# Kernel tuning notes

Measured on AMD Instinct MI355X. Metric: run time of the kernel, lower is better.

## Reference

```python
import jax, jax.numpy as jnp
import numpy as np

E, H, F = 8, 1024, 2048   # experts, hidden, ffn
B, S = 1, 1024
JITTER = 0.01             # router_jitter_noise


def setup_inputs() -> dict:
    key = jax.random.key(0)
    ks = jax.random.split(key, 5)
    return {
        "hidden_states": jax.random.normal(ks[0], (B, S, H), jnp.float32),
        "gate_w": jax.random.normal(ks[1], (E, H), jnp.float32) * 0.02,
        "w1": jax.random.normal(ks[2], (E, F, H), jnp.float32) * 0.02,
        "w2": jax.random.normal(ks[3], (E, H, F), jnp.float32) * 0.02,
        "w3": jax.random.normal(ks[4], (E, F, H), jnp.float32) * 0.02,
    }


def _sparsemixer_eval(scores, jitter_eps):
    # scores: [T, E]. Inference path of sparsemixer (training=False).
    T = scores.shape[0]
    rows = jnp.arange(T)
    # top-1
    max1 = jnp.max(scores, axis=-1, keepdims=True)
    sel1 = jnp.argmax(scores, axis=-1)
    factor1 = jnp.maximum(jnp.abs(scores), max1)          # scores.abs().clamp(min=max1)
    mask1 = (max1 - scores) / factor1 > 2.0 * jitter_eps
    gates1 = jax.nn.softmax(jnp.where(mask1, -jnp.inf, scores), axis=-1)
    mult1 = gates1[rows, sel1]
    # top-2: mask out the top-1 expert
    masked_scores = scores.at[rows, sel1].set(-jnp.inf)
    max2 = jnp.max(masked_scores, axis=-1, keepdims=True)
    sel2 = jnp.argmax(masked_scores, axis=-1)
    factor2 = jnp.maximum(jnp.abs(scores), max2)
    mask2 = (max2 - scores) / factor2 > 2.0 * jitter_eps
    gates2 = jax.nn.softmax(jnp.where(mask2, -jnp.inf, masked_scores), axis=-1)
    mult2 = gates2[rows, sel2]
    multiplier = jnp.stack([mult1, mult2], axis=-1)       # [T, 2]
    selected = jnp.stack([sel1, sel2], axis=-1)           # [T, 2]
    return multiplier, selected


def reference(hidden_states, gate_w, w1, w2, w3):
    b, s, h = hidden_states.shape
    x = hidden_states.reshape(-1, h)                      # [T, H]
    router_logits = x @ gate_w.T                          # [T, E]
    mult, sel = _sparsemixer_eval(router_logits, JITTER)
    n_exp = gate_w.shape[0]
    # combined routing weight per (token, expert): sum of top-k multipliers
    weight = jnp.sum(mult[..., None] * jax.nn.one_hot(sel, n_exp, dtype=x.dtype), axis=1)  # [T, E]
    # dense masked dispatch: evaluate every expert, combine with routing weights
    h1 = jnp.einsum('th,efh->etf', x, w1)                 # [E, T, F]
    h3 = jnp.einsum('th,efh->etf', x, w3)
    inter = jax.nn.silu(h1) * h3
    out_e = jnp.einsum('etf,ehf->eth', inter, w2)         # [E, T, H]
    final = jnp.einsum('eth,te->th', out_e, weight)       # [T, H]
    return final.reshape(b, s, h), router_logits
```

## Files before the change

kernel.cpp:

```cpp
#include <hip/hip_runtime.h>
#include <hip/hip_bf16.h>
#include <math.h>


#define T_TOK 1024
#define H_DIM 1024
#define F_DIM 2048
#define N_EXP 8
#define JIT 0.01f

#define BK  64
#define LDK 68
#define NK1 (H_DIM / BK)
#define NK2 (F_DIM / BK)
#define MT_MAX 24

typedef __bf16 bf16_t;
typedef __bf16 bf16x8 __attribute__((ext_vector_type(8)));
typedef __bf16 bf16x4 __attribute__((ext_vector_type(4)));
typedef float f32x4 __attribute__((ext_vector_type(4)));

__device__ inline bf16x4 cvt4(float4 v) {
    bf16x4 r;
    r[0] = (bf16_t)v.x; r[1] = (bf16_t)v.y; r[2] = (bf16_t)v.z; r[3] = (bf16_t)v.w;
    return r;
}

#define WS_CNT   0
#define WS_BASE  64
#define WS_TOK   128
#define WS_WGT   (128 + 32768)
#define WS_SLOT  (WS_WGT + 32768)
#define WS_INTER 131072
#define WS_ACC   (131072 + 8388608)

__global__ __launch_bounds__(256) void router_k(
    const float* __restrict__ x, const float* __restrict__ gw,
    float* __restrict__ logits_out,
    int* __restrict__ cnt, int* __restrict__ tok,
    float* __restrict__ wgt, int* __restrict__ slot)
{
    int wave = threadIdx.x >> 6, lane = threadIdx.x & 63;
    int t = blockIdx.x * 4 + wave;
    const float* xr = x + (size_t)t * H_DIM;
    int h0 = lane * 16;

    float acc[N_EXP];
#pragma unroll
    for (int e = 0; e < N_EXP; e++) acc[e] = 0.f;
#pragma unroll
    for (int j = 0; j < 16; j += 4) {
        float4 xv = *(const float4*)(xr + h0 + j);
#pragma unroll
        for (int e = 0; e < N_EXP; e++) {
            float4 gv = *(const float4*)(gw + e * H_DIM + h0 + j);
            acc[e] += xv.x * gv.x + xv.y * gv.y + xv.z * gv.z + xv.w * gv.w;
        }
    }
#pragma unroll
    for (int m = 32; m > 0; m >>= 1)
#pragma unroll
        for (int e = 0; e < N_EXP; e++) acc[e] += __shfl_xor(acc[e], m, 64);

    if (lane == 0) {
        float s[N_EXP];
#pragma unroll
        for (int e = 0; e < N_EXP; e++) {
            s[e] = acc[e];
            logits_out[t * N_EXP + e] = s[e];
        }
        float max1 = -INFINITY; int sel1 = 0;
        for (int e = 0; e < N_EXP; e++) if (s[e] > max1) { max1 = s[e]; sel1 = e; }
        float denom1 = 0.f;
        for (int e = 0; e < N_EXP; e++) {
            float factor = fmaxf(fabsf(s[e]), max1);
            bool m = ((max1 - s[e]) / factor) > (2.0f * JIT);
            if (!m) denom1 += expf(s[e] - max1);
        }
        float mult1 = 1.0f / denom1;
        float max2 = -INFINITY; int sel2 = 0;
        for (int e = 0; e < N_EXP; e++)
            if (e != sel1 && s[e] > max2) { max2 = s[e]; sel2 = e; }
        float denom2 = 0.f;
        for (int e = 0; e < N_EXP; e++) {
            if (e == sel1) continue;
            float factor = fmaxf(fabsf(s[e]), max2);
            bool m = ((max2 - s[e]) / factor) > (2.0f * JIT);
            if (!m) denom2 += expf(s[e] - max2);
        }
        float mult2 = 1.0f / denom2;

        int p1 = atomicAdd(&cnt[sel1], 1);
        tok[sel1 * T_TOK + p1] = t; wgt[sel1 * T_TOK + p1] = mult1; slot[sel1 * T_TOK + p1] = 0;
        int p2 = atomicAdd(&cnt[sel2], 1);
        tok[sel2 * T_TOK + p2] = t; wgt[sel2 * T_TOK + p2] = mult2; slot[sel2 * T_TOK + p2] = 1;
    }
}

__global__ void prefix_k(const int* __restrict__ cnt, int* __restrict__ base)
{
    if (threadIdx.x == 0 && blockIdx.x == 0) {
        int a = 0;
        for (int e = 0; e < N_EXP; e++) { base[e] = a; a += cnt[e]; }
    }
}

__global__ __launch_bounds__(256, 2) void gemm1_k(
    const float* __restrict__ x,
    const float* __restrict__ w1,
    const float* __restrict__ w3,
    const int* __restrict__ cnt, const int* __restrict__ base,
    const int* __restrict__ tok,
    bf16_t* __restrict__ inter)
{
    int mt = blockIdx.x >> 5;
    int nt = blockIdx.x & 31;
    int e = 0, m0 = 0, found = 0, accb = 0;
#pragma unroll
    for (int ee = 0; ee < N_EXP; ee++) {
        int b = (cnt[ee] + 127) >> 7;
        if (!found && mt < accb + b) { e = ee; m0 = (mt - accb) << 7; found = 1; }
        accb += b;
    }
    if (!found) return;
    int cntE = cnt[e];
    int n0 = nt * 64;
    int tid = threadIdx.x;
    int lane = tid & 63, quad = lane >> 4, l16 = lane & 15;
    int wave = tid >> 6;

    __shared__ __align__(16) bf16_t Al[2][128 * LDK];
    __shared__ __align__(16) bf16_t B1l[2][64 * LDK];
    __shared__ __align__(16) bf16_t B3l[2][64 * LDK];
    __shared__ int tokL[128];

    if (tid < 128) {
        int r = m0 + tid;
        tokL[tid] = tok[e * T_TOK + (r < cntE ? r : cntE - 1)];
    }
    __syncthreads();

    int rA[8], kA[8], ofsA[8];
#pragma unroll
    for (int i = 0; i < 8; i++) {
        int c = tid + i * 256;
        rA[i] = c >> 4; kA[i] = c & 15;
        ofsA[i] = tokL[rA[i]] * H_DIM + kA[i] * 4;
    }
    int rB[4], kB[4], ofsB[4];
    const float* w1e = w1 + (size_t)e * F_DIM * H_DIM;
    const float* w3e = w3 + (size_t)e * F_DIM * H_DIM;
#pragma unroll
    for (int i = 0; i < 4; i++) {
        int c = tid + i * 256;
        rB[i] = c >> 4; kB[i] = c & 15;
        ofsB[i] = (n0 + rB[i]) * H_DIM + kB[i] * 4;
    }

    f32x4 acc1[2][4], acc3[2][4];
#pragma unroll
    for (int fi = 0; fi < 2; fi++)
#pragma unroll
        for (int fj = 0; fj < 4; fj++) {
            acc1[fi][fj] = f32x4{0.f, 0.f, 0.f, 0.f};
            acc3[fi][fj] = f32x4{0.f, 0.f, 0.f, 0.f};
        }

    float4 pA[8], p1[4], p3[4];
#pragma unroll
    for (int i = 0; i < 8; i++) pA[i] = *(const float4*)(x + ofsA[i]);
#pragma unroll
    for (int i = 0; i < 4; i++) {
        p1[i] = *(const float4*)(w1e + ofsB[i]);
        p3[i] = *(const float4*)(w3e + ofsB[i]);
    }

#pragma unroll 2
    for (int kk = 0; kk < NK1; kk++) {
        const int cur = kk & 1;
#pragma unroll
        for (int i = 0; i < 8; i++)
            *(bf16x4*)&Al[cur][rA[i] * LDK + kA[i] * 4] = cvt4(pA[i]);
#pragma unroll
        for (int i = 0; i < 4; i++) {
            *(bf16x4*)&B1l[cur][rB[i] * LDK + kB[i] * 4] = cvt4(p1[i]);
            *(bf16x4*)&B3l[cur][rB[i] * LDK + kB[i] * 4] = cvt4(p3[i]);
        }
        __syncthreads();
        if (kk + 1 < NK1) {
            const int k0 = (kk + 1) * BK;
#pragma unroll
            for (int i = 0; i < 8; i++) pA[i] = *(const float4*)(x + ofsA[i] + k0);
#pragma unroll
            for (int i = 0; i < 4; i++) {
                p1[i] = *(const float4*)(w1e + ofsB[i] + k0);
                p3[i] = *(const float4*)(w3e + ofsB[i] + k0);
            }
        }
#pragma unroll
        for (int s = 0; s < 2; s++) {
            int ko = s * 32 + quad * 8;
            bf16x8 af[2], b1f[4], b3f[4];
#pragma unroll
            for (int fi = 0; fi < 2; fi++)
                af[fi] = *(const bf16x8*)&Al[cur][(wave * 32 + fi * 16 + l16) * LDK + ko];
#pragma unroll
            for (int fj = 0; fj < 4; fj++) {
                b1f[fj] = *(const bf16x8*)&B1l[cur][(fj * 16 + l16) * LDK + ko];
                b3f[fj] = *(const bf16x8*)&B3l[cur][(fj * 16 + l16) * LDK + ko];
            }
#pragma unroll
            for (int fi = 0; fi < 2; fi++)
#pragma unroll
                for (int fj = 0; fj < 4; fj++) {
                    acc1[fi][fj] = __builtin_amdgcn_mfma_f32_16x16x32_bf16(af[fi], b1f[fj], acc1[fi][fj], 0, 0, 0);
                    acc3[fi][fj] = __builtin_amdgcn_mfma_f32_16x16x32_bf16(af[fi], b3f[fj], acc3[fi][fj], 0, 0, 0);
                }
        }
    }

    int rowBase = base[e];
#pragma unroll
    for (int fi = 0; fi < 2; fi++)
#pragma unroll
        for (int fj = 0; fj < 4; fj++) {
            int ff = n0 + fj * 16 + l16;
#pragma unroll
            for (int r = 0; r < 4; r++) {
                int mm = m0 + wave * 32 + fi * 16 + quad * 4 + r;
                if (mm < cntE) {
                    float h1 = acc1[fi][fj][r], h3 = acc3[fi][fj][r];
                    float v = (h1 / (1.f + expf(-h1))) * h3;
                    inter[(size_t)(rowBase + mm) * F_DIM + ff] = (bf16_t)v;
                }
            }
        }
}

__global__ __launch_bounds__(256, 3) void gemm2_k(
    const bf16_t* __restrict__ inter,
    const float* __restrict__ w2,
    const int* __restrict__ cnt, const int* __restrict__ base,
    const int* __restrict__ tok,
    const float* __restrict__ wgt, const int* __restrict__ slot,
    float* __restrict__ accOut)
{
    int mt = blockIdx.x >> 4;
    int nt = blockIdx.x & 15;
    int e = 0, m0 = 0, found = 0, accb = 0;
#pragma unroll
    for (int ee = 0; ee < N_EXP; ee++) {
        int b = (cnt[ee] + 127) >> 7;
        if (!found && mt < accb + b) { e = ee; m0 = (mt - accb) << 7; found = 1; }
        accb += b;
    }
    if (!found) return;
    int cntE = cnt[e];
    int n0 = nt * 64;
    int tid = threadIdx.x;
    int lane = tid & 63, quad = lane >> 4, l16 = lane & 15;
    int wave = tid >> 6;
    int rowBase = base[e];

    __shared__ __align__(16) bf16_t Al[2][128 * LDK];
    __shared__ __align__(16) bf16_t Bl[2][64 * LDK];

    int rA[4], kA[4], ofsA[4];
#pragma unroll
    for (int i = 0; i < 4; i++) {
        int c = tid + i * 256;
        rA[i] = c >> 3; kA[i] = c & 7;
        int row = m0 + rA[i]; if (row >= cntE) row = cntE - 1;
        ofsA[i] = (rowBase + row) * F_DIM + kA[i] * 8;
    }
    int rB[4], kB[4], ofsB[4];
    const float* w2e = w2 + (size_t)e * H_DIM * F_DIM;
#pragma unroll
    for (int i = 0; i < 4; i++) {
        int c = tid + i * 256;
        rB[i] = c >> 4; kB[i] = c & 15;
        ofsB[i] = (n0 + rB[i]) * F_DIM + kB[i] * 4;
    }

    f32x4 acc[2][4];
#pragma unroll
    for (int fi = 0; fi < 2; fi++)
#pragma unroll
        for (int fj = 0; fj < 4; fj++) acc[fi][fj] = f32x4{0.f, 0.f, 0.f, 0.f};

    bf16x8 pa[4];
    float4 pb[4];
#pragma unroll
    for (int i = 0; i < 4; i++) {
        pa[i] = *(const bf16x8*)(inter + ofsA[i]);
        pb[i] = *(const float4*)(w2e + ofsB[i]);
    }

#pragma unroll 2
    for (int kk = 0; kk < NK2; kk++) {
        const int cur = kk & 1;
#pragma unroll
        for (int i = 0; i < 4; i++) {
            *(bf16x8*)&Al[cur][rA[i] * LDK + kA[i] * 8] = pa[i];
            *(bf16x4*)&Bl[cur][rB[i] * LDK + kB[i] * 4] = cvt4(pb[i]);
        }
        __syncthreads();
        if (kk + 1 < NK2) {
            const int k0 = (kk + 1) * BK;
#pragma unroll
            for (int i = 0; i < 4; i++) {
                pa[i] = *(const bf16x8*)(inter + ofsA[i] + k0);
                pb[i] = *(const float4*)(w2e + ofsB[i] + k0);
            }
        }
#pragma unroll
        for (int s = 0; s < 2; s++) {
            int ko = s * 32 + quad * 8;
            bf16x8 af[2], bfr[4];
#pragma unroll
            for (int fi = 0; fi < 2; fi++)
                af[fi] = *(const bf16x8*)&Al[cur][(wave * 32 + fi * 16 + l16) * LDK + ko];
#pragma unroll
            for (int fj = 0; fj < 4; fj++)
                bfr[fj] = *(const bf16x8*)&Bl[cur][(fj * 16 + l16) * LDK + ko];
#pragma unroll
            for (int fi = 0; fi < 2; fi++)
#pragma unroll
                for (int fj = 0; fj < 4; fj++)
                    acc[fi][fj] = __builtin_amdgcn_mfma_f32_16x16x32_bf16(af[fi], bfr[fj], acc[fi][fj], 0, 0, 0);
        }
    }

#pragma unroll
    for (int fi = 0; fi < 2; fi++)
#pragma unroll
        for (int r = 0; r < 4; r++) {
            int mm = m0 + wave * 32 + fi * 16 + quad * 4 + r;
            if (mm < cntE) {
                int t = tok[e * T_TOK + mm];
                float wv = wgt[e * T_TOK + mm];
                int sl = slot[e * T_TOK + mm];
                float* dst = accOut + (size_t)sl * T_TOK * H_DIM + (size_t)t * H_DIM;
#pragma unroll
                for (int fj = 0; fj < 4; fj++)
                    dst[n0 + fj * 16 + l16] = acc[fi][fj][r] * wv;
            }
        }
}

__global__ __launch_bounds__(256) void combine_k(const float* __restrict__ acc,
                                                 float* __restrict__ out)
{
    int i = blockIdx.x * 256 + threadIdx.x;
    const float4* a0 = (const float4*)acc;
    const float4* a1 = (const float4*)(acc + (size_t)T_TOK * H_DIM);
    float4 v0 = a0[i];
    float4 v1 = a1[i];
    float4 r;
    r.x = v0.x + v1.x; r.y = v0.y + v1.y; r.z = v0.z + v1.z; r.w = v0.w + v1.w;
    ((float4*)out)[i] = r;
}

extern "C" void kernel_launch(void* const* d_in, const int* in_sizes, int n_in,
                              void* d_out, int out_size, void* d_ws, size_t ws_size,
                              hipStream_t stream) {
    const float* x  = (const float*)d_in[0];
    const float* gw = (const float*)d_in[1];
    const float* w1 = (const float*)d_in[2];
    const float* w2 = (const float*)d_in[3];
    const float* w3 = (const float*)d_in[4];
    float* out = (float*)d_out;
    float* logits_out = out + (size_t)T_TOK * H_DIM;

    char* ws = (char*)d_ws;
    int*    cnt   = (int*)(ws + WS_CNT);
    int*    basep = (int*)(ws + WS_BASE);
    int*    tok   = (int*)(ws + WS_TOK);
    float*  wgt   = (float*)(ws + WS_WGT);
    int*    slot  = (int*)(ws + WS_SLOT);
    bf16_t* inter = (bf16_t*)(ws + WS_INTER);
    float*  accO  = (float*)(ws + WS_ACC);

    hipMemsetAsync(cnt, 0, 64, stream);
    router_k<<<T_TOK / 4, 256, 0, stream>>>(x, gw, logits_out, cnt, tok, wgt, slot);
    prefix_k<<<1, 64, 0, stream>>>(cnt, basep);
    gemm1_k<<<dim3(MT_MAX * 32), 256, 0, stream>>>(x, w1, w3, cnt, basep, tok, inter);
    gemm2_k<<<dim3(MT_MAX * 16), 256, 0, stream>>>(inter, w2, cnt, basep, tok, wgt, slot, accO);
    combine_k<<<(T_TOK * H_DIM / 4) / 256, 256, 0, stream>>>(accO, out);
}
```

Before: 314.5 us.

## Stream fp32 weights to LDS via global_load_lds with 4-stage pipeline

Both expert GEMMs now load fp32 weight tiles straight into LDS with global_load_lds, in a four-buffer pipeline that runs two tiles ahead. Each tile is converted to bf16 when read from LDS rather than before storing. Activations (x, inter) are register-prefetched two steps ahead, loaded per wave directly in MFMA fragment layout instead of being staged in LDS. The wave layout changes to a 2x2 grid with 64x32 tiles per wave, and BK drops to 32. gemm2's occupancy hint goes from 3 to 2. The goal is to cut LDS store traffic and register staging and to overlap memory with MFMA, at the cost of hand-tuned vmcnt waits and more LDS use per block.

Measured after the change: 430.8 us. 37.0% more time.

```diff
diff --git a/kernel.cpp b/kernel.cpp
--- a/kernel.cpp
+++ b/kernel.cpp
@@ -9,21 +9,26 @@
 #define N_EXP 8
 #define JIT 0.01f
 
-#define BK  64
-#define LDK 68
+#define BK  32
 #define NK1 (H_DIM / BK)
 #define NK2 (F_DIM / BK)
 #define MT_MAX 24
 
 typedef __bf16 bf16_t;
 typedef __bf16 bf16x8 __attribute__((ext_vector_type(8)));
-typedef __bf16 bf16x4 __attribute__((ext_vector_type(4)));
 typedef float f32x4 __attribute__((ext_vector_type(4)));
 
-__device__ inline bf16x4 cvt4(float4 v) {
-    bf16x4 r;
-    r[0] = (bf16_t)v.x; r[1] = (bf16_t)v.y; r[2] = (bf16_t)v.z; r[3] = (bf16_t)v.w;
+__device__ inline bf16x8 cvt8(float4 a, float4 b) {
+    bf16x8 r;
+    r[0] = (bf16_t)a.x; r[1] = (bf16_t)a.y; r[2] = (bf16_t)a.z; r[3] = (bf16_t)a.w;
+    r[4] = (bf16_t)b.x; r[5] = (bf16_t)b.y; r[6] = (bf16_t)b.z; r[7] = (bf16_t)b.w;
     return r;
+}
+
+__device__ inline void gl16(const float* g, float* l) {
+    __builtin_amdgcn_global_load_lds(
+        (const __attribute__((address_space(1))) unsigned int*)g,
+        (__attribute__((address_space(3))) unsigned int*)l, 16, 0, 0);
 }
 
 #define WS_CNT   0
@@ -128,10 +133,12 @@
     int tid = threadIdx.x;
     int lane = tid & 63, quad = lane >> 4, l16 = lane & 15;
     int wave = tid >> 6;
-
-    __shared__ __align__(16) bf16_t Al[2][128 * LDK];
-    __shared__ __align__(16) bf16_t B1l[2][64 * LDK];
-    __shared__ __align__(16) bf16_t B3l[2][64 * LDK];
+    int wm = wave >> 1, wn = wave & 1;
+
+    __shared__ __align__(16) float Bl0[4096];
+    __shared__ __align__(16) float Bl1[4096];
+    __shared__ __align__(16) float Bl2[4096];
+    __shared__ __align__(16) float Bl3[4096];
     __shared__ int tokL[128];
 
     if (tid < 128) {
@@ -140,96 +147,102 @@
     }
     __syncthreads();
 
-    int rA[8], kA[8], ofsA[8];
-#pragma unroll
-    for (int i = 0; i < 8; i++) {
-        int c = tid + i * 256;
-        rA[i] = c >> 4; kA[i] = c & 15;
-        ofsA[i] = tokL[rA[i]] * H_DIM + kA[i] * 4;
-    }
-    int rB[4], kB[4], ofsB[4];
     const float* w1e = w1 + (size_t)e * F_DIM * H_DIM;
     const float* w3e = w3 + (size_t)e * F_DIM * H_DIM;
-#pragma unroll
-    for (int i = 0; i < 4; i++) {
-        int c = tid + i * 256;
-        rB[i] = c >> 4; kB[i] = c & 15;
-        ofsB[i] = (n0 + rB[i]) * H_DIM + kB[i] * 4;
-    }
-
-    f32x4 acc1[2][4], acc3[2][4];
-#pragma unroll
-    for (int fi = 0; fi < 2; fi++)
-#pragma unroll
-        for (int fj = 0; fj < 4; fj++) {
+
+    const float* srcB[4];
+    int dstF[4];
+#pragma unroll
+    for (int j = 0; j < 4; j++) {
+        int g = wave * 4 + j;
+        int mat = g >> 3, fj = (g >> 1) & 3, h = g & 1;
+        srcB[j] = (mat ? w3e : w1e) + (size_t)(n0 + fj * 16 + l16) * H_DIM + quad * 8 + h * 4;
+        dstF[j] = mat * 2048 + fj * 512 + h * 256;
+    }
+
+    int aoff[4];
+#pragma unroll
+    for (int fi = 0; fi < 4; fi++)
+        aoff[fi] = tokL[wm * 64 + fi * 16 + l16] * H_DIM + quad * 8;
+
+    f32x4 acc1[4][2], acc3[4][2];
+#pragma unroll
+    for (int fi = 0; fi < 4; fi++)
+#pragma unroll
+        for (int fj = 0; fj < 2; fj++) {
             acc1[fi][fj] = f32x4{0.f, 0.f, 0.f, 0.f};
             acc3[fi][fj] = f32x4{0.f, 0.f, 0.f, 0.f};
         }
 
-    float4 pA[8], p1[4], p3[4];
-#pragma unroll
-    for (int i = 0; i < 8; i++) pA[i] = *(const float4*)(x + ofsA[i]);
-#pragma unroll
-    for (int i = 0; i < 4; i++) {
-        p1[i] = *(const float4*)(w1e + ofsB[i]);
-        p3[i] = *(const float4*)(w3e + ofsB[i]);
-    }
-
-#pragma unroll 2
-    for (int kk = 0; kk < NK1; kk++) {
-        const int cur = kk & 1;
-#pragma unroll
-        for (int i = 0; i < 8; i++)
-            *(bf16x4*)&Al[cur][rA[i] * LDK + kA[i] * 4] = cvt4(pA[i]);
-#pragma unroll
-        for (int i = 0; i < 4; i++) {
-            *(bf16x4*)&B1l[cur][rB[i] * LDK + kB[i] * 4] = cvt4(p1[i]);
-            *(bf16x4*)&B3l[cur][rB[i] * LDK + kB[i] * 4] = cvt4(p3[i]);
-        }
-        __syncthreads();
-        if (kk + 1 < NK1) {
-            const int k0 = (kk + 1) * BK;
-#pragma unroll
-            for (int i = 0; i < 8; i++) pA[i] = *(const float4*)(x + ofsA[i] + k0);
-#pragma unroll
-            for (int i = 0; i < 4; i++) {
-                p1[i] = *(const float4*)(w1e + ofsB[i] + k0);
-                p3[i] = *(const float4*)(w3e + ofsB[i] + k0);
-            }
-        }
-#pragma unroll
-        for (int s = 0; s < 2; s++) {
-            int ko = s * 32 + quad * 8;
-            bf16x8 af[2], b1f[4], b3f[4];
-#pragma unroll
-            for (int fi = 0; fi < 2; fi++)
-                af[fi] = *(const bf16x8*)&Al[cur][(wave * 32 + fi * 16 + l16) * LDK + ko];
-#pragma unroll
-            for (int fj = 0; fj < 4; fj++) {
-                b1f[fj] = *(const bf16x8*)&B1l[cur][(fj * 16 + l16) * LDK + ko];
-                b3f[fj] = *(const bf16x8*)&B3l[cur][(fj * 16 + l16) * LDK + ko];
-            }
-#pragma unroll
-            for (int fi = 0; fi < 2; fi++)
-#pragma unroll
-                for (int fj = 0; fj < 4; fj++) {
-                    acc1[fi][fj] = __builtin_amdgcn_mfma_f32_16x16x32_bf16(af[fi], b1f[fj], acc1[fi][fj], 0, 0, 0);
-                    acc3[fi][fj] = __builtin_amdgcn_mfma_f32_16x16x32_bf16(af[fi], b3f[fj], acc3[fi][fj], 0, 0, 0);
-                }
-        }
-    }
+    float4 pa[2][4][2];
+
+#define G1_ISSUE_B(T, WR)                                                   \
+    { _Pragma("unroll") for (int j = 0; j < 4; j++)                         \
+          gl16(srcB[j] + (T) * 32, WR + dstF[j]); }
+
+#define G1_ISSUE_A(T, PAR)                                                  \
+    { _Pragma("unroll") for (int fi = 0; fi < 4; fi++) {                    \
+          pa[PAR][fi][0] = *(const float4*)(x + aoff[fi] + (T) * 32);       \
+          pa[PAR][fi][1] = *(const float4*)(x + aoff[fi] + (T) * 32 + 4); } }
+
+#define G1_SYNC(N)                                                          \
+    __builtin_amdgcn_sched_barrier(0);                                      \
+    asm volatile("s_waitcnt vmcnt(" #N ")" ::: "memory");                   \
+    __builtin_amdgcn_s_barrier();                                           \
+    __builtin_amdgcn_sched_barrier(0);
+
+#define G1_COMPUTE(KK, PAR, RD, DO_A)                                       \
+    {                                                                       \
+        bf16x8 af[4];                                                       \
+        _Pragma("unroll") for (int fi = 0; fi < 4; fi++)                    \
+            af[fi] = cvt8(pa[PAR][fi][0], pa[PAR][fi][1]);                  \
+        if (DO_A) { G1_ISSUE_A((KK) + 2, PAR); }                            \
+        _Pragma("unroll") for (int fjl = 0; fjl < 2; fjl++) {               \
+            int fb = (wn * 2 + fjl) * 512 + lane * 4;                       \
+            float4 u1 = *(const float4*)(RD + fb);                          \
+            float4 v1 = *(const float4*)(RD + fb + 256);                    \
+            float4 u3 = *(const float4*)(RD + 2048 + fb);                   \
+            float4 v3 = *(const float4*)(RD + 2048 + fb + 256);             \
+            bf16x8 b1 = cvt8(u1, v1), b3 = cvt8(u3, v3);                    \
+            _Pragma("unroll") for (int fi = 0; fi < 4; fi++) {              \
+                acc1[fi][fjl] = __builtin_amdgcn_mfma_f32_16x16x32_bf16(af[fi], b1, acc1[fi][fjl], 0, 0, 0); \
+                acc3[fi][fjl] = __builtin_amdgcn_mfma_f32_16x16x32_bf16(af[fi], b3, acc3[fi][fjl], 0, 0, 0); \
+            }                                                               \
+        }                                                                   \
+    }
+
+#define G1_BODY(KK, PAR, WR, RD, N, DO_B, DO_A)                             \
+    { if (DO_B) { G1_ISSUE_B((KK) + 2, WR); }                               \
+      G1_SYNC(N)                                                            \
+      G1_COMPUTE(KK, PAR, RD, DO_A) }
+
+    G1_ISSUE_B(0, Bl0);
+    G1_ISSUE_A(0, 0);
+    G1_ISSUE_B(1, Bl1);
+    G1_ISSUE_A(1, 1);
+
+    for (int kb = 0; kb < 28; kb += 4) {
+        G1_BODY(kb + 0, 0, Bl2, Bl0, 16, 1, 1)
+        G1_BODY(kb + 1, 1, Bl3, Bl1, 16, 1, 1)
+        G1_BODY(kb + 2, 0, Bl0, Bl2, 16, 1, 1)
+        G1_BODY(kb + 3, 1, Bl1, Bl3, 16, 1, 1)
+    }
+    G1_BODY(28, 0, Bl2, Bl0, 16, 1, 1)
+    G1_BODY(29, 1, Bl3, Bl1, 16, 1, 1)
+    G1_BODY(30, 0, Bl0, Bl2, 12, 0, 0)
+    G1_BODY(31, 1, Bl1, Bl3, 0, 0, 0)
 
     int rowBase = base[e];
 #pragma unroll
-    for (int fi = 0; fi < 2; fi++)
-#pragma unroll
-        for (int fj = 0; fj < 4; fj++) {
-            int ff = n0 + fj * 16 + l16;
+    for (int fi = 0; fi < 4; fi++)
+#pragma unroll
+        for (int fjl = 0; fjl < 2; fjl++) {
+            int ff = n0 + wn * 32 + fjl * 16 + l16;
 #pragma unroll
             for (int r = 0; r < 4; r++) {
-                int mm = m0 + wave * 32 + fi * 16 + quad * 4 + r;
+                int mm = m0 + wm * 64 + fi * 16 + quad * 4 + r;
                 if (mm < cntE) {
-                    float h1 = acc1[fi][fj][r], h3 = acc3[fi][fj][r];
+                    float h1 = acc1[fi][fjl][r], h3 = acc3[fi][fjl][r];
                     float v = (h1 / (1.f + expf(-h1))) * h3;
                     inter[(size_t)(rowBase + mm) * F_DIM + ff] = (bf16_t)v;
                 }
@@ -237,7 +250,7 @@
         }
 }
 
-__global__ __launch_bounds__(256, 3) void gemm2_k(
+__global__ __launch_bounds__(256, 2) void gemm2_k(
     const bf16_t* __restrict__ inter,
     const float* __restrict__ w2,
     const int* __restrict__ cnt, const int* __restrict__ base,
@@ -260,90 +273,99 @@
     int tid = threadIdx.x;
     int lane = tid & 63, quad = lane >> 4, l16 = lane & 15;
     int wave = tid >> 6;
+    int wm = wave >> 1, wn = wave & 1;
     int rowBase = base[e];
 
-    __shared__ __align__(16) bf16_t Al[2][128 * LDK];
-    __shared__ __align__(16) bf16_t Bl[2][64 * LDK];
-
-    int rA[4], kA[4], ofsA[4];
-#pragma unroll
-    for (int i = 0; i < 4; i++) {
-        int c = tid + i * 256;
-        rA[i] = c >> 3; kA[i] = c & 7;
-        int row = m0 + rA[i]; if (row >= cntE) row = cntE - 1;
-        ofsA[i] = (rowBase + row) * F_DIM + kA[i] * 8;
-    }
-    int rB[4], kB[4], ofsB[4];
+    __shared__ __align__(16) float Cl0[2048];
+    __shared__ __align__(16) float Cl1[2048];
+    __shared__ __align__(16) float Cl2[2048];
+    __shared__ __align__(16) float Cl3[2048];
+
     const float* w2e = w2 + (size_t)e * H_DIM * F_DIM;
-#pragma unroll
-    for (int i = 0; i < 4; i++) {
-        int c = tid + i * 256;
-        rB[i] = c >> 4; kB[i] = c & 15;
-        ofsB[i] = (n0 + rB[i]) * F_DIM + kB[i] * 4;
-    }
-
-    f32x4 acc[2][4];
-#pragma unroll
-    for (int fi = 0; fi < 2; fi++)
-#pragma unroll
-        for (int fj = 0; fj < 4; fj++) acc[fi][fj] = f32x4{0.f, 0.f, 0.f, 0.f};
-
-    bf16x8 pa[4];
-    float4 pb[4];
-#pragma unroll
-    for (int i = 0; i < 4; i++) {
-        pa[i] = *(const bf16x8*)(inter + ofsA[i]);
-        pb[i] = *(const float4*)(w2e + ofsB[i]);
-    }
-
-#pragma unroll 2
-    for (int kk = 0; kk < NK2; kk++) {
-        const int cur = kk & 1;
-#pragma unroll
-        for (int i = 0; i < 4; i++) {
-            *(bf16x8*)&Al[cur][rA[i] * LDK + kA[i] * 8] = pa[i];
-            *(bf16x4*)&Bl[cur][rB[i] * LDK + kB[i] * 4] = cvt4(pb[i]);
-        }
-        __syncthreads();
-        if (kk + 1 < NK2) {
-            const int k0 = (kk + 1) * BK;
-#pragma unroll
-            for (int i = 0; i < 4; i++) {
-                pa[i] = *(const bf16x8*)(inter + ofsA[i] + k0);
-                pb[i] = *(const float4*)(w2e + ofsB[i] + k0);
-            }
-        }
-#pragma unroll
-        for (int s = 0; s < 2; s++) {
-            int ko = s * 32 + quad * 8;
-            bf16x8 af[2], bfr[4];
-#pragma unroll
-            for (int fi = 0; fi < 2; fi++)
-                af[fi] = *(const bf16x8*)&Al[cur][(wave * 32 + fi * 16 + l16) * LDK + ko];
-#pragma unroll
-            for (int fj = 0; fj < 4; fj++)
-                bfr[fj] = *(const bf16x8*)&Bl[cur][(fj * 16 + l16) * LDK + ko];
-#pragma unroll
-            for (int fi = 0; fi < 2; fi++)
-#pragma unroll
-                for (int fj = 0; fj < 4; fj++)
-                    acc[fi][fj] = __builtin_amdgcn_mfma_f32_16x16x32_bf16(af[fi], bfr[fj], acc[fi][fj], 0, 0, 0);
-        }
-    }
-
-#pragma unroll
-    for (int fi = 0; fi < 2; fi++)
+
+    const float* srcB[2];
+    int dstF[2];
+#pragma unroll
+    for (int j = 0; j < 2; j++) {
+        int g = wave * 2 + j;
+        int fj = g >> 1, h = g & 1;
+        srcB[j] = w2e + (size_t)(n0 + fj * 16 + l16) * F_DIM + quad * 8 + h * 4;
+        dstF[j] = fj * 512 + h * 256;
+    }
+
+    int aoff[4];
+#pragma unroll
+    for (int fi = 0; fi < 4; fi++) {
+        int rr = m0 + wm * 64 + fi * 16 + l16;
+        if (rr >= cntE) rr = cntE - 1;
+        aoff[fi] = (rowBase + rr) * F_DIM + quad * 8;
+    }
+
+    f32x4 acc[4][2];
+#pragma unroll
+    for (int fi = 0; fi < 4; fi++)
+#pragma unroll
+        for (int fj = 0; fj < 2; fj++) acc[fi][fj] = f32x4{0.f, 0.f, 0.f, 0.f};
+
+    bf16x8 pa[2][4];
+
+#define G2_ISSUE_B(T, WR)                                                   \
+    { _Pragma("unroll") for (int j = 0; j < 2; j++)                         \
+          gl16(srcB[j] + (T) * 32, WR + dstF[j]); }
+
+#define G2_ISSUE_A(T, PAR)                                                  \
+    { _Pragma("unroll") for (int fi = 0; fi < 4; fi++)                      \
+          pa[PAR][fi] = *(const bf16x8*)(inter + aoff[fi] + (T) * 32); }
+
+#define G2_COMPUTE(KK, PAR, RD, DO_A)                                       \
+    {                                                                       \
+        bf16x8 af[4];                                                       \
+        _Pragma("unroll") for (int fi = 0; fi < 4; fi++) af[fi] = pa[PAR][fi]; \
+        if (DO_A) { G2_ISSUE_A((KK) + 2, PAR); }                            \
+        _Pragma("unroll") for (int fjl = 0; fjl < 2; fjl++) {               \
+            int fb = (wn * 2 + fjl) * 512 + lane * 4;                       \
+            float4 u = *(const float4*)(RD + fb);                           \
+            float4 v = *(const float4*)(RD + fb + 256);                     \
+            bf16x8 bfr = cvt8(u, v);                                        \
+            _Pragma("unroll") for (int fi = 0; fi < 4; fi++)                \
+                acc[fi][fjl] = __builtin_amdgcn_mfma_f32_16x16x32_bf16(af[fi], bfr, acc[fi][fjl], 0, 0, 0); \
+        }                                                                   \
+    }
+
+#define G2_BODY(KK, PAR, WR, RD, N, DO_B, DO_A)                             \
+    { if (DO_B) { G2_ISSUE_B((KK) + 2, WR); }                               \
+      G1_SYNC(N)                                                            \
+      G2_COMPUTE(KK, PAR, RD, DO_A) }
+
+    G2_ISSUE_B(0, Cl0);
+    G2_ISSUE_A(0, 0);
+    G2_ISSUE_B(1, Cl1);
+    G2_ISSUE_A(1, 1);
+
+    for (int kb = 0; kb < 60; kb += 4) {
+        G2_BODY(kb + 0, 0, Cl2, Cl0, 8, 1, 1)
+        G2_BODY(kb + 1, 1, Cl3, Cl1, 8, 1, 1)
+        G2_BODY(kb + 2, 0, Cl0, Cl2, 8, 1, 1)
+        G2_BODY(kb + 3, 1, Cl1, Cl3, 8, 1, 1)
+    }
+    G2_BODY(60, 0, Cl2, Cl0, 8, 1, 1)
+    G2_BODY(61, 1, Cl3, Cl1, 8, 1, 1)
+    G2_BODY(62, 0, Cl0, Cl2, 6, 0, 0)
+    G2_BODY(63, 1, Cl1, Cl3, 0, 0, 0)
+
+#pragma unroll
+    for (int fi = 0; fi < 4; fi++)
 #pragma unroll
         for (int r = 0; r < 4; r++) {
-            int mm = m0 + wave * 32 + fi * 16 + quad * 4 + r;
+            int mm = m0 + wm * 64 + fi * 16 + quad * 4 + r;
             if (mm < cntE) {
                 int t = tok[e * T_TOK + mm];
                 float wv = wgt[e * T_TOK + mm];
                 int sl = slot[e * T_TOK + mm];
                 float* dst = accOut + (size_t)sl * T_TOK * H_DIM + (size_t)t * H_DIM;
 #pragma unroll
-                for (int fj = 0; fj < 4; fj++)
-                    dst[n0 + fj * 16 + l16] = acc[fi][fj][r] * wv;
+                for (int fjl = 0; fjl < 2; fjl++)
+                    dst[n0 + wn * 32 + fjl * 16 + l16] = acc[fi][fjl][r] * wv;
             }
         }
 }
```
